# Kernel optimization log

Hardware: AMD Instinct MI355X
Metric: run time of the kernel (lower is better)

The kernel has to match this reference:

```python
import jax, jax.numpy as jnp
import numpy as np

NUM_HEADS = 16
HEAD_DIM = 64
MAX_MEM = 4 * 4096
TOP_K = 8
EPS = 1e-8


def _l2norm(x, eps=EPS):
    # matches torch F.normalize(p=2, dim=-1, eps): x / max(||x||, eps)
    n = jnp.sqrt(jnp.sum(x * x, axis=-1, keepdims=True))
    return x / jnp.maximum(n, eps)


def setup_inputs() -> dict:
    key0 = jax.random.key(0)
    ks = jax.random.split(key0, 8)
    B, S, D = 2, 512, 1024
    H, hd = NUM_HEADS, HEAD_DIM
    return {
        "inputs": jax.random.normal(ks[0], (B, S, D), dtype=jnp.float32),
        "query": jax.random.normal(ks[1], (B, H, S, hd), dtype=jnp.float32),
        "key": jax.random.normal(ks[2], (B, H, S, hd), dtype=jnp.float32),
        "value": jax.random.normal(ks[3], (B, H, S, hd), dtype=jnp.float32),
        "outputs": jax.random.normal(ks[4], (B, H, S, hd), dtype=jnp.float32),
        "gate": jnp.zeros((H,), dtype=jnp.float32),  # nn.Parameter init zeros
        "key_memories": jax.random.normal(ks[5], (H, MAX_MEM, hd), dtype=jnp.float32),
        "value_memories": jax.random.normal(ks[6], (H, MAX_MEM, hd), dtype=jnp.float32),
    }


def reference(inputs, query, key, value, outputs, gate, key_memories, value_memories):
    B, S, _ = inputs.shape
    H = query.shape[1]
    hd = HEAD_DIM

    # [B,H,S,d] -> [H, B*S, d]
    q = jnp.transpose(query, (1, 0, 2, 3)).reshape(H, B * S, hd)

    # --- KNN lookup (no_grad in original) ---
    qn = _l2norm(q)                    # [H, N, d]
    kn = _l2norm(key_memories)         # [H, M, d]
    sims = jnp.einsum("hnd,hmd->hnm", qn, kn) / jnp.sqrt(jnp.float32(hd))
    scores, indices = jax.lax.top_k(sims, TOP_K)  # [H, N, k]

    # gather memory values per head: [H, N, k, d]
    mem_vals = jax.vmap(lambda vm, ix: vm[ix])(value_memories, indices)

    # weighted sum over k neighbors
    weighted = jnp.sum(mem_vals * scores[..., None], axis=2)  # [H, N, d]
    weighted = weighted.reshape(H, B, S, hd).transpose(1, 0, 2, 3)  # [B,H,S,d]

    g = jax.nn.sigmoid(gate).reshape(1, H, 1, 1)
    out_dim = outputs.shape[-1]
    combined = g * weighted[..., :out_dim] + (1.0 - g) * outputs
    return combined
```

## Files before the change

kernel.cpp:

```cpp
#include <hip/hip_runtime.h>
#include <math.h>

#define NHEADS 16
#define HD 64
#define MMEM 16384
#define NQ 1024
#define SEQ 512
#define EPS 1e-8f
#define NPART 16
#define NT 32
#define NGRP 32
#define CMAX 8

typedef short bf16x8 __attribute__((ext_vector_type(8)));
typedef float f32x16 __attribute__((ext_vector_type(16)));

__device__ inline unsigned short f2bf(float f) {
    unsigned int u = __builtin_bit_cast(unsigned int, f);
    unsigned int r = (u + 0x7FFFu + ((u >> 16) & 1u)) >> 16;
    return (unsigned short)r;
}

#define SS(Q) (Q.x*Q.x + Q.y*Q.y + Q.z*Q.z + Q.w*Q.w)

__global__ __launch_bounds__(256)
void kprep_kernel(const float* __restrict__ kmem,
                  float* __restrict__ knr,
                  unsigned short* __restrict__ kbf) {
    __shared__ float ssl[256];
    const int tid = threadIdx.x;
    const int gid = blockIdx.x * 256 + tid;
    const int lane = gid & 63;
    const int ks   = (gid >> 6) & 3;
    const int t    = (gid >> 8) & 511;
    const int h    = gid >> 17;
    const int r    = lane & 31;
    const int hi   = lane >> 5;
    const int row  = t * 32 + r;
    const int d0   = ks * 16 + hi * 8;

    const float* src = kmem + (((size_t)h * MMEM + row) << 6) + d0;
    float4 v0 = *(const float4*)(src);
    float4 v1 = *(const float4*)(src + 4);
    ssl[tid] = SS(v0) + SS(v1);
    __syncthreads();
    float tot = ssl[r +   0] + ssl[r +  32] + ssl[r +  64] + ssl[r +  96]
              + ssl[r + 128] + ssl[r + 160] + ssl[r + 192] + ssl[r + 224];
    const float rn = 1.0f / fmaxf(sqrtf(tot), EPS);
    if (tid < 32) knr[h * MMEM + row] = rn;

    uint4 o;
    o.x = (unsigned)f2bf(v0.x * rn) | ((unsigned)f2bf(v0.y * rn) << 16);
    o.y = (unsigned)f2bf(v0.z * rn) | ((unsigned)f2bf(v0.w * rn) << 16);
    o.z = (unsigned)f2bf(v1.x * rn) | ((unsigned)f2bf(v1.y * rn) << 16);
    o.w = (unsigned)f2bf(v1.z * rn) | ((unsigned)f2bf(v1.w * rn) << 16);
    *(uint4*)(kbf + (size_t)gid * 8) = o;
}

__device__ inline float max16v(const f32x16& a) {
    float m0 = fmaxf(fmaxf(a[0],  a[1]),  a[2]);
    float m1 = fmaxf(fmaxf(a[3],  a[4]),  a[5]);
    float m2 = fmaxf(fmaxf(a[6],  a[7]),  a[8]);
    float m3 = fmaxf(fmaxf(a[9],  a[10]), a[11]);
    float m4 = fmaxf(fmaxf(a[12], a[13]), a[14]);
    float n0 = fmaxf(fmaxf(m0, m1), m2);
    float n1 = fmaxf(fmaxf(m3, m4), a[15]);
    return fmaxf(n0, n1);
}

__device__ inline void ins8(float (&tv)[8], float v) {
#pragma unroll
    for (int j = 0; j < 8; ++j) {
        float h_ = fmaxf(tv[j], v);
        float l_ = fminf(tv[j], v);
        tv[j] = h_;
        v = l_;
    }
}

__device__ inline void ins8u64(unsigned long long (&tv)[8], unsigned long long v) {
#pragma unroll
    for (int j = 0; j < 8; ++j) {
        unsigned long long h_ = tv[j] > v ? tv[j] : v;
        unsigned long long l_ = tv[j] > v ? v : tv[j];
        tv[j] = h_;
        v = l_;
    }
}

__device__ inline bf16x8 pack8f(float4 a, float4 b) {
    bf16x8 f;
    f[0] = (short)f2bf(a.x); f[1] = (short)f2bf(a.y);
    f[2] = (short)f2bf(a.z); f[3] = (short)f2bf(a.w);
    f[4] = (short)f2bf(b.x); f[5] = (short)f2bf(b.y);
    f[6] = (short)f2bf(b.z); f[7] = (short)f2bf(b.w);
    return f;
}

#define MFMA4Z(ACC, A0, A1, A2, A3)                                           \
    f32x16 ACC = __builtin_amdgcn_mfma_f32_32x32x16_bf16(A0, qA[0], z16, 0,0,0); \
    ACC = __builtin_amdgcn_mfma_f32_32x32x16_bf16(A1, qA[1], ACC, 0, 0, 0);   \
    ACC = __builtin_amdgcn_mfma_f32_32x32x16_bf16(A2, qA[2], ACC, 0, 0, 0);   \
    ACC = __builtin_amdgcn_mfma_f32_32x32x16_bf16(A3, qA[3], ACC, 0, 0, 0);

__global__ __launch_bounds__(64, 5)
void scanA_kernel(const float* __restrict__ query,
                  const unsigned short* __restrict__ kbf,
                  float* __restrict__ pmax) {
    const int lane = threadIdx.x;
    int bid = blockIdx.x;
    const int p  = bid & 15;  bid >>= 4;
    const int qg = bid & 31;  bid >>= 5;
    const int h  = bid;
    const int col = lane & 31;
    const int hi  = lane >> 5;
    const int n   = qg * 32 + col;

    bf16x8 qA[4];
    {
        const int b0 = n >> 9, s0 = n & 511;
        const float* qp = query + ((((size_t)b0 * NHEADS + h) * SEQ + s0) << 6);
#pragma unroll
        for (int ks = 0; ks < 4; ++ks) {
            const int d0 = ks * 16 + hi * 8;
            qA[ks] = pack8f(*(const float4*)(qp + d0), *(const float4*)(qp + d0 + 4));
        }
    }

    const f32x16 z16 = {0,0,0,0,0,0,0,0,0,0,0,0,0,0,0,0};
    float g = -1e30f;

    const unsigned char* ptr = (const unsigned char*)kbf
        + ((size_t)h * 512 + (size_t)p * NT) * 4096 + (size_t)lane * 16;

    bf16x8 aX0, aX1, aX2, aX3, aY0, aY1, aY2, aY3;
    aX0 = *(const bf16x8*)(ptr);
    aX1 = *(const bf16x8*)(ptr + 1024);
    aX2 = *(const bf16x8*)(ptr + 2048);
    aX3 = *(const bf16x8*)(ptr + 3072);

#pragma unroll 1
    for (int t = 0; t < NT; t += 2) {
        {
            const unsigned char* pn = ptr + (size_t)(t + 1) * 4096;
            aY0 = *(const bf16x8*)(pn);
            aY1 = *(const bf16x8*)(pn + 1024);
            aY2 = *(const bf16x8*)(pn + 2048);
            aY3 = *(const bf16x8*)(pn + 3072);
        }
        {
            MFMA4Z(acc, aX0, aX1, aX2, aX3)
            g = fmaxf(g, max16v(acc));
        }
        if (t + 2 < NT) {
            const unsigned char* p2 = ptr + (size_t)(t + 2) * 4096;
            aX0 = *(const bf16x8*)(p2);
            aX1 = *(const bf16x8*)(p2 + 1024);
            aX2 = *(const bf16x8*)(p2 + 2048);
            aX3 = *(const bf16x8*)(p2 + 3072);
        }
        {
            MFMA4Z(acc2, aY0, aY1, aY2, aY3)
            g = fmaxf(g, max16v(acc2));
        }
    }

    pmax[(((size_t)h * NQ + n) << 5) + p * 2 + hi] = g;
}

__global__ __launch_bounds__(256)
void taured_kernel(const float* __restrict__ pmax,
                   float* __restrict__ tauv) {
    const int gid = blockIdx.x * 256 + threadIdx.x;
    float tv[8];
#pragma unroll
    for (int j = 0; j < 8; ++j) tv[j] = -1e30f;
#pragma unroll
    for (int k = 0; k < NGRP; ++k) ins8(tv, pmax[((size_t)gid << 5) + k]);
    tauv[gid] = tv[7];
}

__global__ __launch_bounds__(64, 5)
void scanB_kernel(const float* __restrict__ query,
                  const unsigned short* __restrict__ kbf,
                  const float* __restrict__ tauv,
                  unsigned* __restrict__ pcand,
                  unsigned* __restrict__ pcnt) {
    const int lane = threadIdx.x;
    int bid = blockIdx.x;
    const int p  = bid & 15;  bid >>= 4;
    const int qg = bid & 31;  bid >>= 5;
    const int h  = bid;
    const int col = lane & 31;
    const int hi  = lane >> 5;
    const int n   = qg * 32 + col;

    bf16x8 qA[4];
    float ssq = 0.f;
    {
        const int b0 = n >> 9, s0 = n & 511;
        const float* qp = query + ((((size_t)b0 * NHEADS + h) * SEQ + s0) << 6);
#pragma unroll
        for (int ks = 0; ks < 4; ++ks) {
            const int d0 = ks * 16 + hi * 8;
            float4 a = *(const float4*)(qp + d0);
            float4 b = *(const float4*)(qp + d0 + 4);
            ssq += SS(a) + SS(b);
            qA[ks] = pack8f(a, b);
        }
    }
    ssq += __shfl_xor(ssq, 32);
    const float tau = tauv[h * NQ + n] - (sqrtf(ssq) * 0.0078125f + 0.01f);

    const f32x16 z16 = {0,0,0,0,0,0,0,0,0,0,0,0,0,0,0,0};

    const unsigned char* ptr = (const unsigned char*)kbf
        + ((size_t)h * 512 + (size_t)p * NT) * 4096 + (size_t)lane * 16;

    unsigned c = 0;
    const size_t ch = (((size_t)h * NQ + n) << 5) + p * 2 + hi;
    unsigned* mpt = pcand + ch * CMAX;

#define EMITG(ACC, MBV) do {                                                  \
        const float _g = max16v(ACC);                                         \
        if (_g >= tau) {                                                      \
            unsigned _msk = 0;                                                \
            _Pragma("unroll")                                                 \
            for (int _r = 0; _r < 16; ++_r)                                   \
                _msk |= (ACC[_r] >= tau) ? (1u << _r) : 0u;                   \
            do {                                                              \
                int _r = __ffs(_msk) - 1;                                     \
                unsigned _idx = (unsigned)((MBV) + (_r & 3) + 8 * (_r >> 2)); \
                if (c < CMAX) mpt[c] = _idx;                                  \
                ++c;                                                          \
                _msk &= _msk - 1;                                             \
            } while (_msk);                                                   \
        }                                                                     \
    } while (0)

    bf16x8 aX0, aX1, aX2, aX3, aY0, aY1, aY2, aY3;
    aX0 = *(const bf16x8*)(ptr);
    aX1 = *(const bf16x8*)(ptr + 1024);
    aX2 = *(const bf16x8*)(ptr + 2048);
    aX3 = *(const bf16x8*)(ptr + 3072);

#pragma unroll 1
    for (int t = 0; t < NT; t += 2) {
        {
            const unsigned char* pn = ptr + (size_t)(t + 1) * 4096;
            aY0 = *(const bf16x8*)(pn);
            aY1 = *(const bf16x8*)(pn + 1024);
            aY2 = *(const bf16x8*)(pn + 2048);
            aY3 = *(const bf16x8*)(pn + 3072);
        }
        {
            MFMA4Z(acc, aX0, aX1, aX2, aX3)
            EMITG(acc, p * 1024 + t * 32 + 4 * hi);
        }
        if (t + 2 < NT) {
            const unsigned char* p2 = ptr + (size_t)(t + 2) * 4096;
            aX0 = *(const bf16x8*)(p2);
            aX1 = *(const bf16x8*)(p2 + 1024);
            aX2 = *(const bf16x8*)(p2 + 2048);
            aX3 = *(const bf16x8*)(p2 + 3072);
        }
        {
            MFMA4Z(acc2, aY0, aY1, aY2, aY3)
            EMITG(acc2, p * 1024 + (t + 1) * 32 + 4 * hi);
        }
    }
    pcnt[ch] = c;
#undef EMITG
}

__global__ __launch_bounds__(64, 8)
void rescore_merge_kernel(const float* __restrict__ query,
                          const float* __restrict__ kmem,
                          const float* __restrict__ knr,
                          const unsigned* __restrict__ pcand,
                          const unsigned* __restrict__ pcnt,
                          const float* __restrict__ vmem,
                          const float* __restrict__ outputs,
                          const float* __restrict__ gate,
                          float* __restrict__ out) {
    __shared__ unsigned cands[NGRP * CMAX];
    const int gid = blockIdx.x;
    const int h = gid >> 10;
    const int n = gid & 1023;
    const int b = n >> 9;
    const int s = n & 511;
    const int lane = threadIdx.x;
    const int d4 = lane & 15;
    const int d5 = lane & 31;

    const float* qbase = query + ((((size_t)b * NHEADS + h) * SEQ + s) << 6);
    const float4 q4 = ((const float4*)qbase)[d4];
    float ssp = SS(q4);
    ssp += __shfl_xor(ssp, 1);
    ssp += __shfl_xor(ssp, 2);
    ssp += __shfl_xor(ssp, 4);
    ssp += __shfl_xor(ssp, 8);
    const float qs = 1.0f / (fmaxf(sqrtf(ssp), EPS) * 8.0f);

    const unsigned cg = pcnt[((size_t)gid << 5) + d5];
    const bool anyovf = (__ballot(cg > CMAX) != 0ULL);
    unsigned inc = cg;
#pragma unroll
    for (int d = 1; d < 32; d <<= 1) {
        unsigned t = __shfl_up(inc, d, 32);
        if (d5 >= d) inc += t;
    }
    const unsigned ct = __shfl(inc, 31, 32);
    const unsigned excl = inc - cg;
    if (lane < 32) {
        const unsigned* lp = pcand + (((size_t)gid << 5) + lane) * CMAX;
        const unsigned cc = cg > CMAX ? CMAX : cg;
        for (unsigned c = 0; c < cc; ++c) cands[excl + c] = lp[c];
    }
    __syncthreads();

    const float* kb = kmem + ((size_t)h << 20);
    const float* nb = knr + h * MMEM;

    unsigned long long top[8];
#pragma unroll
    for (int j = 0; j < 8; ++j) top[j] = 0ULL;

#define SCORE_KEY(IDX) ({                                                     \
        float4 kv = ((const float4*)(kb + ((size_t)(IDX) << 6)))[d4];         \
        float d = q4.x*kv.x + q4.y*kv.y + q4.z*kv.z + q4.w*kv.w;              \
        d += __shfl_xor(d, 1);                                                \
        d += __shfl_xor(d, 2);                                                \
        d += __shfl_xor(d, 4);                                                \
        d += __shfl_xor(d, 8);                                                \
        const float sc = d * qs * nb[IDX];                                    \
        unsigned su = __builtin_bit_cast(unsigned, sc);                       \
        unsigned ms = su ^ ((su >> 31) ? 0xFFFFFFFFu : 0x80000000u);          \
        ((unsigned long long)ms << 32) | (0xFFFFFFFFu - (unsigned)(IDX));     \
    })

    if (!anyovf) {
#pragma unroll 1
        for (unsigned c = 0; c < ct; ++c) {
            const unsigned idx = cands[c];
            ins8u64(top, SCORE_KEY(idx));
        }
    } else {
#pragma unroll 1
        for (int m = 0; m < MMEM; ++m) ins8u64(top, SCORE_KEY(m));
    }
#undef SCORE_KEY

    float acc = 0.0f;
    const float* vb = vmem + ((size_t)h << 20);
#pragma unroll
    for (int j = 0; j < 8; ++j) {
        const unsigned long long key = top[j];
        const unsigned idx = 0xFFFFFFFFu - (unsigned)(key & 0xFFFFFFFFu);
        const unsigned ms = (unsigned)(key >> 32);
        const unsigned su = ms ^ ((ms >> 31) ? 0x80000000u : 0xFFFFFFFFu);
        const float sc = __builtin_bit_cast(float, su);
        acc = fmaf(sc, vb[((size_t)idx << 6) + lane], acc);
    }

    const float gg = 1.0f / (1.0f + expf(-gate[h]));
    const size_t off = ((((size_t)b * NHEADS + h) * SEQ + s) << 6) + lane;
    out[off] = gg * acc + (1.0f - gg) * outputs[off];
}

__global__ void knorm_kernel(const float* __restrict__ kmem,
                             float* __restrict__ knr) {
    int gid = blockIdx.x * 256 + threadIdx.x;
    int mem = gid >> 4;
    int d4  = gid & 15;
    float4 kv = reinterpret_cast<const float4*>(kmem)[(size_t)mem * 16 + d4];
    float ss = SS(kv);
    ss += __shfl_xor(ss, 1);
    ss += __shfl_xor(ss, 2);
    ss += __shfl_xor(ss, 4);
    ss += __shfl_xor(ss, 8);
    if (d4 == 0) knr[mem] = 1.0f / fmaxf(sqrtf(ss), EPS);
}

__global__ __launch_bounds__(64, 4)
void scan_kernel(const float* __restrict__ query,
                 const float* __restrict__ kmem,
                 const float* __restrict__ knr,
                 float* __restrict__ pscore,
                 int* __restrict__ pidx,
                 int P, int CH) {
    const int lane = threadIdx.x & 63;
    int bid = blockIdx.x;
    const int p  = bid % P;  bid /= P;
    const int qb = bid & 15; bid >>= 4;
    const int h  = bid;
    const int n  = qb * 64 + lane;
    const int b  = n >> 9;
    const int s  = n & 511;

    const float4* qp = reinterpret_cast<const float4*>(
        query + (((size_t)b * NHEADS + h) * SEQ + s) * HD);
    float q[HD];
    float ss = 0.0f;
#pragma unroll
    for (int i = 0; i < 16; ++i) {
        float4 v = qp[i];
        q[4*i+0] = v.x; q[4*i+1] = v.y; q[4*i+2] = v.z; q[4*i+3] = v.w;
        ss += SS(v);
    }
    const float rq = 1.0f / (fmaxf(sqrtf(ss), EPS) * 8.0f);
#pragma unroll
    for (int i = 0; i < HD; ++i) q[i] *= rq;

    float tv[8]; int ti[8];
#pragma unroll
    for (int j = 0; j < 8; ++j) { tv[j] = -INFINITY; ti[j] = 0; }

    const int m0 = p * CH;
    const float4* kp = reinterpret_cast<const float4*>(
        kmem + ((size_t)h * MMEM + m0) * HD);
    const float* knrp = knr + h * MMEM + m0;

    for (int mm = 0; mm < CH; ++mm) {
        float d0 = 0.f, d1 = 0.f, d2 = 0.f, d3 = 0.f;
#pragma unroll
        for (int i = 0; i < 16; ++i) {
            float4 kv = kp[(size_t)mm * 16 + i];
            d0 = fmaf(q[4*i+0], kv.x, d0);
            d1 = fmaf(q[4*i+1], kv.y, d1);
            d2 = fmaf(q[4*i+2], kv.z, d2);
            d3 = fmaf(q[4*i+3], kv.w, d3);
        }
        const float sim = ((d0 + d1) + (d2 + d3)) * knrp[mm];
        if (sim > tv[7]) {
            tv[7] = sim; ti[7] = m0 + mm;
#pragma unroll
            for (int j = 7; j > 0; --j) {
                if (tv[j] > tv[j-1]) {
                    float tf = tv[j]; tv[j] = tv[j-1]; tv[j-1] = tf;
                    int   tu = ti[j]; ti[j] = ti[j-1]; ti[j-1] = tu;
                }
            }
        }
    }

    const size_t base = (((size_t)h * NQ + n) * P + p) * 8;
#pragma unroll
    for (int j = 0; j < 8; ++j) { pscore[base+j] = tv[j]; pidx[base+j] = ti[j]; }
}

__global__ void merge_kernel(const float* __restrict__ pscore,
                             const int* __restrict__ pidx,
                             const float* __restrict__ vmem,
                             const float* __restrict__ outputs,
                             const float* __restrict__ gate,
                             float* __restrict__ out, int P) {
    const int t = blockIdx.x * 256 + threadIdx.x;
    const int h = t >> 10;
    const int n = t & 1023;
    const int b = n >> 9;
    const int s = n & 511;

    float tv[8]; int ti[8];
    const size_t base = ((size_t)h * NQ + n) * P * 8;
#pragma unroll
    for (int j = 0; j < 8; ++j) { tv[j] = pscore[base + j]; ti[j] = pidx[base + j]; }
    const int total = P * 8;
    for (int c = 8; c < total; ++c) {
        const float v = pscore[base + c];
        if (v > tv[7]) {
            tv[7] = v; ti[7] = pidx[base + c];
#pragma unroll
            for (int j = 7; j > 0; --j) {
                if (tv[j] > tv[j-1]) {
                    float tf = tv[j]; tv[j] = tv[j-1]; tv[j-1] = tf;
                    int   tu = ti[j]; ti[j] = ti[j-1]; ti[j-1] = tu;
                }
            }
        }
    }

    float4 acc[16];
#pragma unroll
    for (int i = 0; i < 16; ++i) acc[i] = make_float4(0.f, 0.f, 0.f, 0.f);
#pragma unroll
    for (int j = 0; j < 8; ++j) {
        const float4* vp = reinterpret_cast<const float4*>(
            vmem + ((size_t)h * MMEM + ti[j]) * HD);
        const float sc = tv[j];
#pragma unroll
        for (int i = 0; i < 16; ++i) {
            float4 v = vp[i];
            acc[i].x = fmaf(sc, v.x, acc[i].x);
            acc[i].y = fmaf(sc, v.y, acc[i].y);
            acc[i].z = fmaf(sc, v.z, acc[i].z);
            acc[i].w = fmaf(sc, v.w, acc[i].w);
        }
    }

    const float g  = 1.0f / (1.0f + expf(-gate[h]));
    const float og = 1.0f - g;
    const size_t off = (((size_t)b * NHEADS + h) * SEQ + s) * HD;
    const float4* op = reinterpret_cast<const float4*>(outputs + off);
    float4* dst = reinterpret_cast<float4*>(out + off);
#pragma unroll
    for (int i = 0; i < 16; ++i) {
        float4 o = op[i];
        float4 r;
        r.x = g * acc[i].x + og * o.x;
        r.y = g * acc[i].y + og * o.y;
        r.z = g * acc[i].z + og * o.z;
        r.w = g * acc[i].w + og * o.w;
        dst[i] = r;
    }
}

extern "C" void kernel_launch(void* const* d_in, const int* in_sizes, int n_in,
                              void* d_out, int out_size, void* d_ws, size_t ws_size,
                              hipStream_t stream) {
    const float* query   = (const float*)d_in[1];
    const float* outputs = (const float*)d_in[4];
    const float* gate    = (const float*)d_in[5];
    const float* kmem    = (const float*)d_in[6];
    const float* vmem    = (const float*)d_in[7];
    float* out = (float*)d_out;

    const size_t NQTOT    = (size_t)NHEADS * NQ;
    const size_t sz_knr   = (size_t)NHEADS * MMEM * 4;
    const size_t sz_kbf   = (size_t)NHEADS * MMEM * HD * 2;
    const size_t sz_pmax  = NQTOT * NGRP * 4;
    const size_t sz_tauv  = NQTOT * 4;
    const size_t sz_pcand = NQTOT * NGRP * CMAX * 4;
    const size_t sz_pcnt  = NQTOT * NGRP * 4;
    const size_t need = sz_knr + sz_kbf + sz_pmax + sz_tauv + sz_pcand + sz_pcnt;

    if (ws_size >= need) {
        char* w = (char*)d_ws;
        float*          knr   = (float*)w;          w += sz_knr;
        unsigned short* kbf   = (unsigned short*)w; w += sz_kbf;
        float*          pmax  = (float*)w;          w += sz_pmax;
        float*          tauv  = (float*)w;          w += sz_tauv;
        unsigned*       pcand = (unsigned*)w;       w += sz_pcand;
        unsigned*       pcnt  = (unsigned*)w;

        kprep_kernel<<<(NHEADS * 512 * 4 * 64) / 256, 256, 0, stream>>>(kmem, knr, kbf);
        scanA_kernel<<<NHEADS * 32 * NPART, 64, 0, stream>>>(query, kbf, pmax);
        taured_kernel<<<(int)(NQTOT / 256), 256, 0, stream>>>(pmax, tauv);
        scanB_kernel<<<NHEADS * 32 * NPART, 64, 0, stream>>>(query, kbf, tauv, pcand, pcnt);
        rescore_merge_kernel<<<(int)NQTOT, 64, 0, stream>>>(
            query, kmem, knr, pcand, pcnt, vmem, outputs, gate, out);
    } else {
        int P = 16;
        while (P > 4 &&
               (size_t)NHEADS * MMEM * 4 + (size_t)NHEADS * NQ * (size_t)P * 64 > ws_size)
            P >>= 1;
        const int CH = MMEM / P;

        float* knr    = (float*)d_ws;
        float* pscore = knr + (size_t)NHEADS * MMEM;
        int*   pidx   = (int*)(pscore + (size_t)NHEADS * NQ * (size_t)P * 8);

        knorm_kernel<<<(NHEADS * MMEM * 16) / 256, 256, 0, stream>>>(kmem, knr);
        scan_kernel<<<NHEADS * 16 * P, 64, 0, stream>>>(
            query, kmem, knr, pscore, pidx, P, CH);
        merge_kernel<<<(NHEADS * NQ) / 256, 256, 0, stream>>>(
            pscore, pidx, vmem, outputs, gate, out, P);
    }
}
```

Before: 161.2 us.

## Process two 32-query tiles per wave in scan kernels to reuse key loads

Each wave in scanA and scanB now handles 64 queries instead of 32, running two MFMA accumulator chains against the same loaded bf16 key fragments. This halves global key traffic per query and halves the grid size, and the launch-bounds occupancy hint drops from 5 to 4 waves. The cost is more registers per wave, fewer waves to hide latency, and lower parallelism (4096 blocks instead of 8192).

```diff
diff --git a/kernel.cpp b/kernel.cpp
--- a/kernel.cpp
+++ b/kernel.cpp
@@ -97,38 +97,46 @@
     return f;
 }
 
-#define MFMA4Z(ACC, A0, A1, A2, A3)                                           \
-    f32x16 ACC = __builtin_amdgcn_mfma_f32_32x32x16_bf16(A0, qA[0], z16, 0,0,0); \
-    ACC = __builtin_amdgcn_mfma_f32_32x32x16_bf16(A1, qA[1], ACC, 0, 0, 0);   \
-    ACC = __builtin_amdgcn_mfma_f32_32x32x16_bf16(A2, qA[2], ACC, 0, 0, 0);   \
-    ACC = __builtin_amdgcn_mfma_f32_32x32x16_bf16(A3, qA[3], ACC, 0, 0, 0);
-
-__global__ __launch_bounds__(64, 5)
+#define MFMA8Z(ACCA, ACCB, A0, A1, A2, A3)                                    \
+    f32x16 ACCA = __builtin_amdgcn_mfma_f32_32x32x16_bf16(A0, qA[0], z16, 0,0,0); \
+    f32x16 ACCB = __builtin_amdgcn_mfma_f32_32x32x16_bf16(A0, qB[0], z16, 0,0,0); \
+    ACCA = __builtin_amdgcn_mfma_f32_32x32x16_bf16(A1, qA[1], ACCA, 0, 0, 0); \
+    ACCB = __builtin_amdgcn_mfma_f32_32x32x16_bf16(A1, qB[1], ACCB, 0, 0, 0); \
+    ACCA = __builtin_amdgcn_mfma_f32_32x32x16_bf16(A2, qA[2], ACCA, 0, 0, 0); \
+    ACCB = __builtin_amdgcn_mfma_f32_32x32x16_bf16(A2, qB[2], ACCB, 0, 0, 0); \
+    ACCA = __builtin_amdgcn_mfma_f32_32x32x16_bf16(A3, qA[3], ACCA, 0, 0, 0); \
+    ACCB = __builtin_amdgcn_mfma_f32_32x32x16_bf16(A3, qB[3], ACCB, 0, 0, 0);
+
+__global__ __launch_bounds__(64, 4)
 void scanA_kernel(const float* __restrict__ query,
                   const unsigned short* __restrict__ kbf,
                   float* __restrict__ pmax) {
     const int lane = threadIdx.x;
     int bid = blockIdx.x;
     const int p  = bid & 15;  bid >>= 4;
-    const int qg = bid & 31;  bid >>= 5;
+    const int qg = bid & 15;  bid >>= 4;
     const int h  = bid;
     const int col = lane & 31;
     const int hi  = lane >> 5;
-    const int n   = qg * 32 + col;
-
-    bf16x8 qA[4];
+    const int n0  = qg * 64 + col;
+    const int n1  = n0 + 32;
+
+    bf16x8 qA[4], qB[4];
     {
-        const int b0 = n >> 9, s0 = n & 511;
-        const float* qp = query + ((((size_t)b0 * NHEADS + h) * SEQ + s0) << 6);
+        const int b0 = n0 >> 9, s0 = n0 & 511;
+        const int b1 = n1 >> 9, s1 = n1 & 511;
+        const float* qp0 = query + ((((size_t)b0 * NHEADS + h) * SEQ + s0) << 6);
+        const float* qp1 = query + ((((size_t)b1 * NHEADS + h) * SEQ + s1) << 6);
 #pragma unroll
         for (int ks = 0; ks < 4; ++ks) {
             const int d0 = ks * 16 + hi * 8;
-            qA[ks] = pack8f(*(const float4*)(qp + d0), *(const float4*)(qp + d0 + 4));
+            qA[ks] = pack8f(*(const float4*)(qp0 + d0), *(const float4*)(qp0 + d0 + 4));
+            qB[ks] = pack8f(*(const float4*)(qp1 + d0), *(const float4*)(qp1 + d0 + 4));
         }
     }
 
     const f32x16 z16 = {0,0,0,0,0,0,0,0,0,0,0,0,0,0,0,0};
-    float g = -1e30f;
+    float gA = -1e30f, gB = -1e30f;
 
     const unsigned char* ptr = (const unsigned char*)kbf
         + ((size_t)h * 512 + (size_t)p * NT) * 4096 + (size_t)lane * 16;
@@ -149,8 +157,9 @@
             aY3 = *(const bf16x8*)(pn + 3072);
         }
         {
-            MFMA4Z(acc, aX0, aX1, aX2, aX3)
-            g = fmaxf(g, max16v(acc));
+            MFMA8Z(accA, accB, aX0, aX1, aX2, aX3)
+            gA = fmaxf(gA, max16v(accA));
+            gB = fmaxf(gB, max16v(accB));
         }
         if (t + 2 < NT) {
             const unsigned char* p2 = ptr + (size_t)(t + 2) * 4096;
@@ -160,12 +169,14 @@
             aX3 = *(const bf16x8*)(p2 + 3072);
         }
         {
-            MFMA4Z(acc2, aY0, aY1, aY2, aY3)
-            g = fmaxf(g, max16v(acc2));
-        }
-    }
-
-    pmax[(((size_t)h * NQ + n) << 5) + p * 2 + hi] = g;
+            MFMA8Z(accC, accD, aY0, aY1, aY2, aY3)
+            gA = fmaxf(gA, max16v(accC));
+            gB = fmaxf(gB, max16v(accD));
+        }
+    }
+
+    pmax[(((size_t)h * NQ + n0) << 5) + p * 2 + hi] = gA;
+    pmax[(((size_t)h * NQ + n1) << 5) + p * 2 + hi] = gB;
 }
 
 __global__ __launch_bounds__(256)
@@ -180,7 +191,7 @@
     tauv[gid] = tv[7];
 }
 
-__global__ __launch_bounds__(64, 5)
+__global__ __launch_bounds__(64, 4)
 void scanB_kernel(const float* __restrict__ query,
                   const unsigned short* __restrict__ kbf,
                   const float* __restrict__ tauv,
@@ -189,50 +200,59 @@
     const int lane = threadIdx.x;
     int bid = blockIdx.x;
     const int p  = bid & 15;  bid >>= 4;
-    const int qg = bid & 31;  bid >>= 5;
+    const int qg = bid & 15;  bid >>= 4;
     const int h  = bid;
     const int col = lane & 31;
     const int hi  = lane >> 5;
-    const int n   = qg * 32 + col;
-
-    bf16x8 qA[4];
-    float ssq = 0.f;
+    const int n0  = qg * 64 + col;
+    const int n1  = n0 + 32;
+
+    bf16x8 qA[4], qB[4];
+    float ssA = 0.f, ssB = 0.f;
     {
-        const int b0 = n >> 9, s0 = n & 511;
-        const float* qp = query + ((((size_t)b0 * NHEADS + h) * SEQ + s0) << 6);
+        const int b0 = n0 >> 9, s0 = n0 & 511;
+        const int b1 = n1 >> 9, s1 = n1 & 511;
+        const float* qp0 = query + ((((size_t)b0 * NHEADS + h) * SEQ + s0) << 6);
+        const float* qp1 = query + ((((size_t)b1 * NHEADS + h) * SEQ + s1) << 6);
 #pragma unroll
         for (int ks = 0; ks < 4; ++ks) {
             const int d0 = ks * 16 + hi * 8;
-            float4 a = *(const float4*)(qp + d0);
-            float4 b = *(const float4*)(qp + d0 + 4);
-            ssq += SS(a) + SS(b);
-            qA[ks] = pack8f(a, b);
-        }
-    }
-    ssq += __shfl_xor(ssq, 32);
-    const float tau = tauv[h * NQ + n] - (sqrtf(ssq) * 0.0078125f + 0.01f);
+            float4 a0 = *(const float4*)(qp0 + d0), b0v = *(const float4*)(qp0 + d0 + 4);
+            float4 a1 = *(const float4*)(qp1 + d0), b1v = *(const float4*)(qp1 + d0 + 4);
+            ssA += SS(a0) + SS(b0v);
+            ssB += SS(a1) + SS(b1v);
+            qA[ks] = pack8f(a0, b0v);
+            qB[ks] = pack8f(a1, b1v);
+        }
+    }
+    ssA += __shfl_xor(ssA, 32);
+    ssB += __shfl_xor(ssB, 32);
+    const float tA = tauv[h * NQ + n0] - (sqrtf(ssA) * 0.0078125f + 0.01f);
+    const float tB = tauv[h * NQ + n1] - (sqrtf(ssB) * 0.0078125f + 0.01f);
 
     const f32x16 z16 = {0,0,0,0,0,0,0,0,0,0,0,0,0,0,0,0};
 
     const unsigned char* ptr = (const unsigned char*)kbf
         + ((size_t)h * 512 + (size_t)p * NT) * 4096 + (size_t)lane * 16;
 
-    unsigned c = 0;
-    const size_t ch = (((size_t)h * NQ + n) << 5) + p * 2 + hi;
-    unsigned* mpt = pcand + ch * CMAX;
-
-#define EMITG(ACC, MBV) do {                                                  \
+    unsigned cA = 0, cB = 0;
+    const size_t chA = (((size_t)h * NQ + n0) << 5) + p * 2 + hi;
+    const size_t chB = (((size_t)h * NQ + n1) << 5) + p * 2 + hi;
+    unsigned* mApt = pcand + chA * CMAX;
+    unsigned* mBpt = pcand + chB * CMAX;
+
+#define EMITG(ACC, TAU, C, LST, MBV) do {                                     \
         const float _g = max16v(ACC);                                         \
-        if (_g >= tau) {                                                      \
+        if (_g >= (TAU)) {                                                    \
             unsigned _msk = 0;                                                \
             _Pragma("unroll")                                                 \
             for (int _r = 0; _r < 16; ++_r)                                   \
-                _msk |= (ACC[_r] >= tau) ? (1u << _r) : 0u;                   \
+                _msk |= (ACC[_r] >= (TAU)) ? (1u << _r) : 0u;                 \
             do {                                                              \
                 int _r = __ffs(_msk) - 1;                                     \
                 unsigned _idx = (unsigned)((MBV) + (_r & 3) + 8 * (_r >> 2)); \
-                if (c < CMAX) mpt[c] = _idx;                                  \
-                ++c;                                                          \
+                if ((C) < CMAX) (LST)[C] = _idx;                              \
+                ++(C);                                                        \
                 _msk &= _msk - 1;                                             \
             } while (_msk);                                                   \
         }                                                                     \
@@ -254,8 +274,10 @@
             aY3 = *(const bf16x8*)(pn + 3072);
         }
         {
-            MFMA4Z(acc, aX0, aX1, aX2, aX3)
-            EMITG(acc, p * 1024 + t * 32 + 4 * hi);
+            MFMA8Z(accA, accB, aX0, aX1, aX2, aX3)
+            const int mbv = p * 1024 + t * 32 + 4 * hi;
+            EMITG(accA, tA, cA, mApt, mbv);
+            EMITG(accB, tB, cB, mBpt, mbv);
         }
         if (t + 2 < NT) {
             const unsigned char* p2 = ptr + (size_t)(t + 2) * 4096;
@@ -265,11 +287,14 @@
             aX3 = *(const bf16x8*)(p2 + 3072);
         }
         {
-            MFMA4Z(acc2, aY0, aY1, aY2, aY3)
-            EMITG(acc2, p * 1024 + (t + 1) * 32 + 4 * hi);
-        }
-    }
-    pcnt[ch] = c;
+            MFMA8Z(accC, accD, aY0, aY1, aY2, aY3)
+            const int mbv = p * 1024 + (t + 1) * 32 + 4 * hi;
+            EMITG(accC, tA, cA, mApt, mbv);
+            EMITG(accD, tB, cB, mBpt, mbv);
+        }
+    }
+    pcnt[chA] = cA;
+    pcnt[chB] = cB;
 #undef EMITG
 }
 
@@ -544,9 +569,9 @@
         unsigned*       pcnt  = (unsigned*)w;
 
         kprep_kernel<<<(NHEADS * 512 * 4 * 64) / 256, 256, 0, stream>>>(kmem, knr, kbf);
-        scanA_kernel<<<NHEADS * 32 * NPART, 64, 0, stream>>>(query, kbf, pmax);
+        scanA_kernel<<<NHEADS * 16 * NPART, 64, 0, stream>>>(query, kbf, pmax);
         taured_kernel<<<(int)(NQTOT / 256), 256, 0, stream>>>(pmax, tauv);
-        scanB_kernel<<<NHEADS * 32 * NPART, 64, 0, stream>>>(query, kbf, tauv, pcand, pcnt);
+        scanB_kernel<<<NHEADS * 16 * NPART, 64, 0, stream>>>(query, kbf, tauv, pcand, pcnt);
         rescore_merge_kernel<<<(int)NQTOT, 64, 0, stream>>>(
             query, kmem, knr, pcand, pcnt, vmem, outputs, gate, out);
     } else {
```

New measurement: 149.7 us. -7.1%, faster.
